# Performance work log

Hardware: AMD Instinct MI355X
Metric: run time of the kernel (lower is better)

The kernel has to match this reference:

```python
import jax, jax.numpy as jnp
import numpy as np

EMBED_LEN = 512
NUM_FEA = 8   # M
NUM_CLS = 14  # C
BETA = 0.3
BATCH = 8192


def setup_inputs() -> dict:
    key = jax.random.key(0)
    k1, k2, k3 = jax.random.split(key, 3)
    x = jax.random.normal(k1, (BATCH, EMBED_LEN * NUM_FEA), dtype=jnp.float32)
    wordvec_array = jax.random.normal(k2, (1, EMBED_LEN, NUM_CLS), dtype=jnp.float32)
    y = jax.random.randint(k3, (BATCH, NUM_CLS), 0, 2, dtype=jnp.int32)
    # guarantee at least one positive and one negative label per sample
    y = y.at[:, 0].set(1).at[:, -1].set(0)
    return {"x": x, "y": y, "wordvec_array": wordvec_array}


def reference(x, y, wordvec_array):
    B = x.shape[0]
    un = x.reshape(B, EMBED_LEN, -1)            # [B, E, M]
    w = wordvec_array[0]                         # [E, C]
    # dot_prod_all[b, c] = max_m <un[b,:,m], w[:,c]>
    dot = jnp.einsum('bem,ec->bmc', un, w).max(axis=1)   # [B, C]

    P = (y == 1).astype(x.dtype)                 # positive mask [B, C]
    N = 1.0 - P                                  # negative mask [B, C]
    npos = P.sum(axis=-1)                        # [B]
    nneg = N.sum(axis=-1)                        # [B]

    # pairwise v[b,p,n] = dot_neg - dot_pos; sum softplus over masked pairs
    V = dot[:, None, :] - dot[:, :, None]        # [B, C(pos), C(neg)]
    pair_sum = jnp.einsum('bp,bn,bpn->b', P, N, jax.nn.softplus(V))
    # edge case: no negatives -> v = -dot_pos
    noneg_sum = jnp.sum(P * jax.nn.softplus(-dot), axis=-1)
    S = jnp.where(nneg > 0, pair_sum, noneg_sum)
    base = S / npos                              # [B]

    # diversity: unbiased variance of positive-class word vectors over class dim
    mean_w = jnp.einsum('bc,ec->be', P, w) / npos[:, None]          # [B, E]
    ss = jnp.einsum('bc,bec->be', P, (w[None] - mean_w[:, :, None]) ** 2)
    var_w = ss / jnp.maximum(npos - 1.0, 1.0)[:, None]
    var_w = jnp.where((npos == 1.0)[:, None], 0.0, var_w)           # sig = 0 if single positive
    total_var = var_w.sum(axis=-1)               # [B]

    # var_regularization: unbiased var over M, L1 over embed dim
    sig2 = jnp.var(un, axis=2, ddof=1)           # [B, E]
    l1_err = jnp.abs(sig2).sum(axis=-1)          # [B]

    # num_fea > 1 branch
    loss = 2.0 * ((1.0 - BETA) * (1.0 + total_var) * base + BETA * l1_err)
    return loss.mean()
```

## Files before the change

### kernel.cpp

```cpp
#include <hip/hip_runtime.h>
#include <math.h>

#define E_LEN 512
#define C_CLS 14
#define BATCH 8192
#define S_PER_BLOCK 4
#define NSLOTS 256

template<int CTRL>
__device__ __forceinline__ float dpp_mov_f(float v) {
  return __int_as_float(__builtin_amdgcn_update_dpp(
      0, __float_as_int(v), CTRL, 0xF, 0xF, false));
}
__device__ __forceinline__ float sum16(float v) {
  v += dpp_mov_f<0x128>(v);
  v += dpp_mov_f<0x124>(v);
  v += dpp_mov_f<0x122>(v);
  v += dpp_mov_f<0x121>(v);
  return v;
}
__device__ __forceinline__ float sum4_16(float v) {
  v += dpp_mov_f<0x128>(v);
  v += dpp_mov_f<0x124>(v);
  return v;
}
__device__ __forceinline__ float max8(float v) {
  v = fmaxf(v, dpp_mov_f<0xB1>(v));
  v = fmaxf(v, dpp_mov_f<0x4E>(v));
  v = fmaxf(v, dpp_mov_f<0x141>(v));
  return v;
}
__device__ __forceinline__ float softplus_f(float v) {
  return fmaxf(v, 0.f) + __logf(1.f + __expf(-fabsf(v)));
}

__global__ void MID_LOSS_prep(const float* __restrict__ w,
                              float* __restrict__ wsf) {
  __shared__ float wl[E_LEN * C_CLS];
  const int tid = threadIdx.x;
#pragma unroll
  for (int i = 0; i < 7; ++i)
    ((float4*)wl)[tid + i * 256] = ((const float4*)w)[tid + i * 256];
  wsf[tid] = 0.f;
  __syncthreads();
  if (tid < 196) {
    const int p = tid / 14, n = tid - p * 14;
    float g = 0.f;
    for (int e = 0; e < E_LEN; ++e)
      g = fmaf(wl[e * 14 + p], wl[e * 14 + n], g);
    wsf[NSLOTS + tid] = g;
  }
}

__global__ __launch_bounds__(256, 3)
void MID_LOSS_main(const float* __restrict__ x, const int* __restrict__ y,
                   const float* __restrict__ w, const float* __restrict__ wsf,
                   float* __restrict__ slots) {
  __shared__ float wp_s[7 * 1024];
  __shared__ float scr[14 * 264];
  __shared__ float var_s[E_LEN * 2];
  __shared__ float G_s[196];
  __shared__ float P_s[C_CLS];
  __shared__ float dot_s[C_CLS];
  __shared__ float pair_scr[16], g_scr[16], l1_scr[8];

  const int tid = threadIdx.x;
  const int lane = tid & 63;
  const int wid = tid >> 6;
  const int mh = wid & 1;
  const int eh = wid >> 1;

#pragma unroll
  for (int i = 0; i < 7; ++i) {
    const int idx = tid + i * 256;
    const float4 v = ((const float4*)w)[idx];
    const float vv[4] = {v.x, v.y, v.z, v.w};
#pragma unroll
    for (int k = 0; k < 4; ++k) {
      const int f = idx * 4 + k;
      const int e = f / 14;
      const int c = f - e * 14;
      wp_s[(c >> 1) * 1024 + e * 2 + (c & 1)] = vv[k];
    }
  }
  if (tid < 196) G_s[tid] = wsf[NSLOTS + tid];

  float block_loss = 0.f;

  for (int s = 0; s < S_PER_BLOCK; ++s) {
    const int b = blockIdx.x * S_PER_BLOCK + s;
    const float* xrow = x + (size_t)b * (E_LEN * 8);

    __syncthreads();
    if (tid < C_CLS) P_s[tid] = (y[b * C_CLS + tid] == 1) ? 1.f : 0.f;

    float U[4][4];
#pragma unroll
    for (int j = 0; j < 4; ++j) {
      const int e = eh * 256 + j * 64 + lane;
      *(float4*)U[j] = *(const float4*)(xrow + e * 8 + mh * 4);
    }
    float vs1[4], vs2[4];
#pragma unroll
    for (int j = 0; j < 4; ++j) {
      float s1 = U[j][0] + U[j][1] + U[j][2] + U[j][3];
      float s2 = U[j][0] * U[j][0];
      s2 = fmaf(U[j][1], U[j][1], s2);
      s2 = fmaf(U[j][2], U[j][2], s2);
      s2 = fmaf(U[j][3], U[j][3], s2);
      vs1[j] = s1;
      vs2[j] = s2;
    }
    if (mh == 1) {
#pragma unroll
      for (int j = 0; j < 4; ++j) {
        const int e = eh * 256 + j * 64 + lane;
        *(float2*)(var_s + e * 2) = make_float2(vs1[j], vs2[j]);
      }
    }
    float acc[14][4];
#pragma unroll
    for (int c = 0; c < 14; ++c)
#pragma unroll
      for (int m = 0; m < 4; ++m) acc[c][m] = 0.f;
#pragma unroll
    for (int j = 0; j < 4; ++j) {
      const int e = eh * 256 + j * 64 + lane;
      const float* wb = wp_s + e * 2;
#pragma unroll
      for (int cp = 0; cp < 7; ++cp) {
        const float2 w2 = *(const float2*)(wb + cp * 1024);
#pragma unroll
        for (int m = 0; m < 4; ++m) {
          acc[2 * cp][m]     = fmaf(U[j][m], w2.x, acc[2 * cp][m]);
          acc[2 * cp + 1][m] = fmaf(U[j][m], w2.y, acc[2 * cp + 1][m]);
        }
      }
    }
#pragma unroll
    for (int c = 0; c < 14; ++c)
#pragma unroll
      for (int m = 0; m < 4; ++m) acc[c][m] = sum4_16(acc[c][m]);
    if ((lane & 15) < 4) {
      const int part = eh * 16 + (lane >> 4) * 4 + (lane & 3);
#pragma unroll
      for (int c = 0; c < 14; ++c)
        *(float4*)(scr + c * 264 + part * 8 + mh * 4) =
            make_float4(acc[c][0], acc[c][1], acc[c][2], acc[c][3]);
    }
    __syncthreads();

    if (mh == 1) {
      const int r = eh * 64 + lane;
      const int craw = r >> 3;
      const int c = (craw > 13) ? 13 : craw;
      const int m = r & 7;
      float dv = 0.f;
#pragma unroll
      for (int p = 0; p < 32; ++p) dv += scr[c * 264 + p * 8 + m];
      dv = max8(dv);
      if ((r & 7) == 0 && craw < 14) dot_s[c] = dv;
    } else {
      float l1 = 0.f;
#pragma unroll
      for (int j = 0; j < 4; ++j) {
        const int e = eh * 256 + j * 64 + lane;
        const float2 o = *(const float2*)(var_s + e * 2);
        const float s1 = vs1[j] + o.x;
        const float s2 = vs2[j] + o.y;
        const float sig = (s2 - s1 * s1 * 0.125f) * (1.f / 7.f);
        l1 += fabsf(sig);
      }
      l1 = sum16(l1);
      if ((lane & 15) == 0) l1_scr[eh * 4 + (lane >> 4)] = l1;
    }
    __syncthreads();

    {
      const int tt = (tid < 196) ? tid : 0;
      const int p = tt / 14;
      const int n = tt - p * 14;
      const float act = (tid < 196) ? 1.f : 0.f;
      const float Pp = P_s[p];
      const float Pn = P_s[n];
      const float v = dot_s[n] - dot_s[p];
      float aP = act * Pp * (1.f - Pn) * softplus_f(v);
      float aG = act * Pp * Pn * G_s[tt];
      aP = sum16(aP);
      aG = sum16(aG);
      if ((lane & 15) == 0) {
        pair_scr[tid >> 4] = aP;
        g_scr[tid >> 4] = aG;
      }
    }
    __syncthreads();

    if (tid == 0) {
      float S = 0.f, sumG = 0.f;
#pragma unroll
      for (int r2 = 0; r2 < 16; ++r2) { S += pair_scr[r2]; sumG += g_scr[r2]; }
      float l1e = 0.f;
#pragma unroll
      for (int r2 = 0; r2 < 8; ++r2) l1e += l1_scr[r2];
      float npos = 0.f;
      for (int c = 0; c < 14; ++c) npos += P_s[c];
      const float nneg = 14.f - npos;
      float base;
      if (nneg > 0.f) {
        base = S / npos;
      } else {
        float t2 = 0.f;
        for (int c = 0; c < 14; ++c)
          if (P_s[c] > 0.5f) t2 += softplus_f(-dot_s[c]);
        base = t2 / npos;
      }
      float sumW2 = 0.f;
      for (int c = 0; c < 14; ++c) sumW2 += P_s[c] * G_s[c * 14 + c];
      float tv = 0.f;
      if (npos > 1.5f) tv = (sumW2 - sumG / npos) / (npos - 1.f);
      block_loss += 1.4f * (1.f + tv) * base + 0.6f * l1e;
    }
  }
  if (tid == 0) atomicAdd(&slots[blockIdx.x & (NSLOTS - 1)], block_loss);
}

__global__ void MID_LOSS_fin(const float* __restrict__ wsf,
                             float* __restrict__ out) {
  __shared__ float r[4];
  const int tid = threadIdx.x;
  float s = wsf[tid] + wsf[tid + 64] + wsf[tid + 128] + wsf[tid + 192];
  s = sum16(s);
  if ((tid & 15) == 0) r[tid >> 4] = s;
  __syncthreads();
  if (tid == 0) out[0] = (r[0] + r[1] + r[2] + r[3]) * (1.f / (float)BATCH);
}

extern "C" void kernel_launch(void* const* d_in, const int* in_sizes, int n_in,
                              void* d_out, int out_size, void* d_ws, size_t ws_size,
                              hipStream_t stream) {
  const float* x = (const float*)d_in[0];
  const int* y = (const int*)d_in[1];
  const float* w = (const float*)d_in[2];
  float* out = (float*)d_out;
  float* wsf = (float*)d_ws;

  MID_LOSS_prep<<<1, 256, 0, stream>>>(w, wsf);
  MID_LOSS_main<<<BATCH / S_PER_BLOCK, 256, 0, stream>>>(x, y, w, wsf, wsf);
  MID_LOSS_fin<<<1, 64, 0, stream>>>(wsf, out);
}
```

Before: 212.4 us.

## Prefetch next sample, use packed FMA, collapse per-sample reductions into one wave

```diff
diff --git a/kernel.cpp b/kernel.cpp
--- a/kernel.cpp
+++ b/kernel.cpp
@@ -6,6 +6,21 @@
 #define BATCH 8192
 #define S_PER_BLOCK 4
 #define NSLOTS 256
+#define SCR_STRIDE 68
+
+typedef float v2f __attribute__((ext_vector_type(2)));
+typedef float v4f __attribute__((ext_vector_type(4)));
+
+#define PK_FMA_LO(acc, u, wv) \
+  asm("v_pk_fma_f32 %0, %1, %2, %0 op_sel_hi:[1,0,1]" : "+v"(acc) : "v"(u), "v"(wv))
+#define PK_FMA_HI(acc, u, wv) \
+  asm("v_pk_fma_f32 %0, %1, %2, %0 op_sel:[0,1,0]" : "+v"(acc) : "v"(u), "v"(wv))
+#define PK_MUL_LO(d, u, wv) \
+  asm("v_pk_mul_f32 %0, %1, %2 op_sel_hi:[1,0]" : "=v"(d) : "v"(u), "v"(wv))
+#define PK_MUL_HI(d, u, wv) \
+  asm("v_pk_mul_f32 %0, %1, %2 op_sel:[0,1]" : "=v"(d) : "v"(u), "v"(wv))
+
+#define BAR() asm volatile("s_waitcnt lgkmcnt(0)\ns_barrier" ::: "memory")
 
 template<int CTRL>
 __device__ __forceinline__ float dpp_mov_f(float v) {
@@ -19,10 +34,14 @@
   v += dpp_mov_f<0x121>(v);
   return v;
 }
-__device__ __forceinline__ float sum4_16(float v) {
-  v += dpp_mov_f<0x128>(v);
-  v += dpp_mov_f<0x124>(v);
+__device__ __forceinline__ float wsum64(float v) {
+  v = sum16(v);
+  v += dpp_mov_f<0x142>(v);
+  v += dpp_mov_f<0x143>(v);
   return v;
+}
+__device__ __forceinline__ float rl63(float v) {
+  return __int_as_float(__builtin_amdgcn_readlane(__float_as_int(v), 63));
 }
 __device__ __forceinline__ float max8(float v) {
   v = fmaxf(v, dpp_mov_f<0xB1>(v));
@@ -52,120 +71,148 @@
   }
 }
 
-__global__ __launch_bounds__(256, 3)
+__global__ __launch_bounds__(256, 4)
 void MID_LOSS_main(const float* __restrict__ x, const int* __restrict__ y,
                    const float* __restrict__ w, const float* __restrict__ wsf,
                    float* __restrict__ slots) {
-  __shared__ float wp_s[7 * 1024];
-  __shared__ float scr[14 * 264];
-  __shared__ float var_s[E_LEN * 2];
+  __shared__ alignas(16) float wp_s[7 * 1024];
+  __shared__ alignas(16) float scr[14 * SCR_STRIDE];
+  __shared__ alignas(8)  float var_s[E_LEN * 2];
   __shared__ float G_s[196];
-  __shared__ float P_s[C_CLS];
+  __shared__ float P4_s[S_PER_BLOCK * C_CLS];
   __shared__ float dot_s[C_CLS];
-  __shared__ float pair_scr[16], g_scr[16], l1_scr[8];
+  __shared__ float l1_scr[8];
+  __shared__ float npos_s[S_PER_BLOCK];
+  __shared__ float w2sum_s[S_PER_BLOCK];
 
   const int tid = threadIdx.x;
   const int lane = tid & 63;
   const int wid = tid >> 6;
   const int mh = wid & 1;
   const int eh = wid >> 1;
+  const int ebase = eh * 256 + lane;
+  const int b0 = blockIdx.x * S_PER_BLOCK;
+
+  alignas(16) v2f U[2][4][2];
+  {
+    const float* xr = x + (size_t)b0 * (E_LEN * 8);
+#pragma unroll
+    for (int j = 0; j < 4; ++j)
+      *(v4f*)&U[0][j][0] = *(const v4f*)(xr + (ebase + j * 64) * 8 + mh * 4);
+  }
 
 #pragma unroll
   for (int i = 0; i < 7; ++i) {
     const int idx = tid + i * 256;
-    const float4 v = ((const float4*)w)[idx];
-    const float vv[4] = {v.x, v.y, v.z, v.w};
+    const v4f v = ((const v4f*)w)[idx];
 #pragma unroll
     for (int k = 0; k < 4; ++k) {
       const int f = idx * 4 + k;
       const int e = f / 14;
       const int c = f - e * 14;
-      wp_s[(c >> 1) * 1024 + e * 2 + (c & 1)] = vv[k];
+      wp_s[(c >> 1) * 1024 + e * 2 + (c & 1)] = v[k];
     }
   }
   if (tid < 196) G_s[tid] = wsf[NSLOTS + tid];
+  if (tid < S_PER_BLOCK * C_CLS)
+    P4_s[tid] = (y[b0 * C_CLS + tid] == 1) ? 1.f : 0.f;
+  BAR();
+  if (tid < S_PER_BLOCK) {
+    float np = 0.f;
+    for (int c = 0; c < C_CLS; ++c) np += P4_s[tid * C_CLS + c];
+    npos_s[tid] = np;
+  } else if (tid < 2 * S_PER_BLOCK) {
+    const int s = tid - S_PER_BLOCK;
+    float sw = 0.f;
+    for (int c = 0; c < C_CLS; ++c)
+      sw = fmaf(P4_s[s * C_CLS + c], G_s[c * 15], sw);
+    w2sum_s[s] = sw;
+  }
+  BAR();
 
   float block_loss = 0.f;
 
+#pragma unroll
   for (int s = 0; s < S_PER_BLOCK; ++s) {
-    const int b = blockIdx.x * S_PER_BLOCK + s;
-    const float* xrow = x + (size_t)b * (E_LEN * 8);
-
-    __syncthreads();
-    if (tid < C_CLS) P_s[tid] = (y[b * C_CLS + tid] == 1) ? 1.f : 0.f;
-
-    float U[4][4];
+    const int cur = s & 1, nxt = cur ^ 1;
+
+    float vs1[4], vs2[4];
 #pragma unroll
     for (int j = 0; j < 4; ++j) {
-      const int e = eh * 256 + j * 64 + lane;
-      *(float4*)U[j] = *(const float4*)(xrow + e * 8 + mh * 4);
-    }
-    float vs1[4], vs2[4];
+      const v2f t = U[cur][j][0] + U[cur][j][1];
+      vs1[j] = t.x + t.y;
+      v2f q = U[cur][j][0] * U[cur][j][0];
+      q += U[cur][j][1] * U[cur][j][1];
+      vs2[j] = q.x + q.y;
+    }
+    if (mh == 1) {
+#pragma unroll
+      for (int j = 0; j < 4; ++j) {
+        v2f o;
+        o.x = vs1[j];
+        o.y = vs2[j];
+        *(v2f*)(var_s + 2 * (ebase + j * 64)) = o;
+      }
+    }
+
+    alignas(16) v2f acc[14][2];
 #pragma unroll
     for (int j = 0; j < 4; ++j) {
-      float s1 = U[j][0] + U[j][1] + U[j][2] + U[j][3];
-      float s2 = U[j][0] * U[j][0];
-      s2 = fmaf(U[j][1], U[j][1], s2);
-      s2 = fmaf(U[j][2], U[j][2], s2);
-      s2 = fmaf(U[j][3], U[j][3], s2);
-      vs1[j] = s1;
-      vs2[j] = s2;
-    }
-    if (mh == 1) {
-#pragma unroll
-      for (int j = 0; j < 4; ++j) {
-        const int e = eh * 256 + j * 64 + lane;
-        *(float2*)(var_s + e * 2) = make_float2(vs1[j], vs2[j]);
-      }
-    }
-    float acc[14][4];
-#pragma unroll
-    for (int c = 0; c < 14; ++c)
-#pragma unroll
-      for (int m = 0; m < 4; ++m) acc[c][m] = 0.f;
-#pragma unroll
-    for (int j = 0; j < 4; ++j) {
-      const int e = eh * 256 + j * 64 + lane;
+      const int e = ebase + j * 64;
       const float* wb = wp_s + e * 2;
 #pragma unroll
       for (int cp = 0; cp < 7; ++cp) {
-        const float2 w2 = *(const float2*)(wb + cp * 1024);
-#pragma unroll
-        for (int m = 0; m < 4; ++m) {
-          acc[2 * cp][m]     = fmaf(U[j][m], w2.x, acc[2 * cp][m]);
-          acc[2 * cp + 1][m] = fmaf(U[j][m], w2.y, acc[2 * cp + 1][m]);
+        const v2f wv = *(const v2f*)(wb + cp * 1024);
+        if (j == 0) {
+          PK_MUL_LO(acc[2 * cp][0], U[cur][0][0], wv);
+          PK_MUL_LO(acc[2 * cp][1], U[cur][0][1], wv);
+          PK_MUL_HI(acc[2 * cp + 1][0], U[cur][0][0], wv);
+          PK_MUL_HI(acc[2 * cp + 1][1], U[cur][0][1], wv);
+        } else {
+          PK_FMA_LO(acc[2 * cp][0], U[cur][j][0], wv);
+          PK_FMA_LO(acc[2 * cp][1], U[cur][j][1], wv);
+          PK_FMA_HI(acc[2 * cp + 1][0], U[cur][j][0], wv);
+          PK_FMA_HI(acc[2 * cp + 1][1], U[cur][j][1], wv);
         }
       }
     }
-#pragma unroll
-    for (int c = 0; c < 14; ++c)
-#pragma unroll
-      for (int m = 0; m < 4; ++m) acc[c][m] = sum4_16(acc[c][m]);
-    if ((lane & 15) < 4) {
-      const int part = eh * 16 + (lane >> 4) * 4 + (lane & 3);
+
+    if (s < S_PER_BLOCK - 1) {
+      const float* xn = x + (size_t)(b0 + s + 1) * (E_LEN * 8);
+#pragma unroll
+      for (int j = 0; j < 4; ++j)
+        *(v4f*)&U[nxt][j][0] = *(const v4f*)(xn + (ebase + j * 64) * 8 + mh * 4);
+    }
+
+#pragma unroll
+    for (int c = 0; c < 14; ++c) {
+      acc[c][0].x = sum16(acc[c][0].x);
+      acc[c][0].y = sum16(acc[c][0].y);
+      acc[c][1].x = sum16(acc[c][1].x);
+      acc[c][1].y = sum16(acc[c][1].y);
+    }
+    if ((lane & 15) == 0) {
+      float* sp = scr + (eh * 4 + (lane >> 4)) * 8 + mh * 4;
 #pragma unroll
       for (int c = 0; c < 14; ++c)
-        *(float4*)(scr + c * 264 + part * 8 + mh * 4) =
-            make_float4(acc[c][0], acc[c][1], acc[c][2], acc[c][3]);
-    }
-    __syncthreads();
+        *(float4*)(sp + c * SCR_STRIDE) = *(float4*)&acc[c][0];
+    }
+    BAR();
 
     if (mh == 1) {
       const int r = eh * 64 + lane;
       const int craw = r >> 3;
       const int c = (craw > 13) ? 13 : craw;
       const int m = r & 7;
-      float dv = 0.f;
-#pragma unroll
-      for (int p = 0; p < 32; ++p) dv += scr[c * 264 + p * 8 + m];
+      const float* sp = scr + c * SCR_STRIDE + m;
+      float dv = sp[0] + sp[8] + sp[16] + sp[24] + sp[32] + sp[40] + sp[48] + sp[56];
       dv = max8(dv);
       if ((r & 7) == 0 && craw < 14) dot_s[c] = dv;
     } else {
       float l1 = 0.f;
 #pragma unroll
       for (int j = 0; j < 4; ++j) {
-        const int e = eh * 256 + j * 64 + lane;
-        const float2 o = *(const float2*)(var_s + e * 2);
+        const v2f o = *(const v2f*)(var_s + 2 * (ebase + j * 64));
         const float s1 = vs1[j] + o.x;
         const float s2 = vs2[j] + o.y;
         const float sig = (s2 - s1 * s1 * 0.125f) * (1.f / 7.f);
@@ -174,50 +221,31 @@
       l1 = sum16(l1);
       if ((lane & 15) == 0) l1_scr[eh * 4 + (lane >> 4)] = l1;
     }
-    __syncthreads();
-
-    {
-      const int tt = (tid < 196) ? tid : 0;
-      const int p = tt / 14;
-      const int n = tt - p * 14;
-      const float act = (tid < 196) ? 1.f : 0.f;
-      const float Pp = P_s[p];
-      const float Pn = P_s[n];
-      const float v = dot_s[n] - dot_s[p];
-      float aP = act * Pp * (1.f - Pn) * softplus_f(v);
-      float aG = act * Pp * Pn * G_s[tt];
-      aP = sum16(aP);
-      aG = sum16(aG);
-      if ((lane & 15) == 0) {
-        pair_scr[tid >> 4] = aP;
-        g_scr[tid >> 4] = aG;
-      }
-    }
-    __syncthreads();
-
-    if (tid == 0) {
-      float S = 0.f, sumG = 0.f;
-#pragma unroll
-      for (int r2 = 0; r2 < 16; ++r2) { S += pair_scr[r2]; sumG += g_scr[r2]; }
-      float l1e = 0.f;
-#pragma unroll
-      for (int r2 = 0; r2 < 8; ++r2) l1e += l1_scr[r2];
-      float npos = 0.f;
-      for (int c = 0; c < 14; ++c) npos += P_s[c];
-      const float nneg = 14.f - npos;
-      float base;
-      if (nneg > 0.f) {
-        base = S / npos;
-      } else {
-        float t2 = 0.f;
-        for (int c = 0; c < 14; ++c)
-          if (P_s[c] > 0.5f) t2 += softplus_f(-dot_s[c]);
-        base = t2 / npos;
-      }
-      float sumW2 = 0.f;
-      for (int c = 0; c < 14; ++c) sumW2 += P_s[c] * G_s[c * 14 + c];
-      float tv = 0.f;
-      if (npos > 1.5f) tv = (sumW2 - sumG / npos) / (npos - 1.f);
+    BAR();
+
+    if (wid == 0) {
+      const float* Pv = P4_s + s * C_CLS;
+      float Sc = 0.f, Gc = 0.f, Lc = 0.f;
+#pragma unroll
+      for (int k = 0; k < 4; ++k) {
+        const int tt = lane + k * 64;
+        if (tt < 196) {
+          const int p = (tt * 2341) >> 15;
+          const int n = tt - p * 14;
+          const float Pp = Pv[p], Pn = Pv[n];
+          Sc += Pp * (1.f - Pn) * softplus_f(dot_s[n] - dot_s[p]);
+          Gc = fmaf(Pp * Pn, G_s[tt], Gc);
+        }
+      }
+      if (lane < 8) Lc = l1_scr[lane];
+      Sc = wsum64(Sc);
+      Gc = wsum64(Gc);
+      Lc = wsum64(Lc);
+      const float S = rl63(Sc), sumG = rl63(Gc), l1e = rl63(Lc);
+      const float npos = npos_s[s];
+      const float base = S / npos;
+      const float tv =
+          (npos > 1.5f) ? (w2sum_s[s] - sumG / npos) / (npos - 1.f) : 0.f;
       block_loss += 1.4f * (1.f + tv) * base + 0.6f * l1e;
     }
   }
@@ -226,13 +254,10 @@
 
 __global__ void MID_LOSS_fin(const float* __restrict__ wsf,
                              float* __restrict__ out) {
-  __shared__ float r[4];
   const int tid = threadIdx.x;
   float s = wsf[tid] + wsf[tid + 64] + wsf[tid + 128] + wsf[tid + 192];
-  s = sum16(s);
-  if ((tid & 15) == 0) r[tid >> 4] = s;
-  __syncthreads();
-  if (tid == 0) out[0] = (r[0] + r[1] + r[2] + r[3]) * (1.f / (float)BATCH);
+  s = wsum64(s);
+  if (tid == 63) out[0] = s * (1.f / (float)BATCH);
 }
 
 extern "C" void kernel_launch(void* const* d_in, const int* in_sizes, int n_in,
```

Measured after the change: 256.5 us. +20.8%, slower.
